# Performance work log

Measured on AMD Instinct MI355X. Metric: run time of the kernel, lower is better.

## Reference

```python
import jax, jax.numpy as jnp
import numpy as np

N_ATOMS = 131072
N_EDGES = 1048576  # avg degree 8
D = 64             # atom_state_dim
H = 64             # hidden width of all MLPs
OUT = 16           # output_dim
ATOMS_PER_MOL = 32
N_MOLS = N_ATOMS // ATOMS_PER_MOL  # 4096


def setup_inputs() -> dict:
    key = jax.random.key(0)
    ks = jax.random.split(key, 16)

    def lin(k, fan_in, fan_out):
        kw, kb = jax.random.split(k)
        bound = 1.0 / np.sqrt(fan_in)
        w = jax.random.uniform(kw, (fan_in, fan_out), jnp.float32, -bound, bound)
        b = jax.random.uniform(kb, (fan_out,), jnp.float32, -bound, bound)
        return w, b

    atom_states = jax.random.normal(ks[0], (N_ATOMS, D), jnp.float32)
    edge_src = jax.random.randint(ks[1], (N_EDGES,), 0, N_ATOMS, jnp.int32)
    edge_dst = jax.random.randint(ks[2], (N_EDGES,), 0, N_ATOMS, jnp.int32)
    atom_seg = (jnp.arange(N_ATOMS, dtype=jnp.int32) // ATOMS_PER_MOL)

    ms0_w, ms0_b = lin(ks[3], 2 * D, H)   # message MLP: 2d -> 64
    ms1_w, ms1_b = lin(ks[4], H, H)       # 64 -> 64
    ms2_w, ms2_b = lin(ks[5], H, D)       # 64 -> d
    fc1_w, fc1_b = lin(ks[6], D, H)       # readout: d -> 64
    fc2_w, fc2_b = lin(ks[7], H, H)       # 64 -> 64
    out_w, out_b = lin(ks[8], H, OUT)     # 64 -> output_dim

    return dict(atom_states=atom_states, edge_src=edge_src, edge_dst=edge_dst,
                atom_seg=atom_seg,
                ms0_w=ms0_w, ms0_b=ms0_b, ms1_w=ms1_w, ms1_b=ms1_b,
                ms2_w=ms2_w, ms2_b=ms2_b, fc1_w=fc1_w, fc1_b=fc1_b,
                fc2_w=fc2_w, fc2_b=fc2_b, out_w=out_w, out_b=out_b)


def reference(atom_states, edge_src, edge_dst, atom_seg,
              ms0_w, ms0_b, ms1_w, ms1_b, ms2_w, ms2_b,
              fc1_w, fc1_b, fc2_w, fc2_b, out_w, out_b):
    # per-edge feature: concat(state[dst_atom], state[neighbor])  -> [E, 2d]
    edge_feat = jnp.concatenate(
        [atom_states[edge_dst], atom_states[edge_src]], axis=-1)
    # message MLP (relu after every layer, as in the torch code)
    m = jax.nn.relu(edge_feat @ ms0_w + ms0_b)
    m = jax.nn.relu(m @ ms1_w + ms1_b)
    m = jax.nn.relu(m @ ms2_w + ms2_b)            # [E, d]
    # sum of incoming messages per atom (torch: stack(messages).sum(0))
    new_states = jax.ops.segment_sum(m, edge_dst, num_segments=N_ATOMS)  # [n_atoms, d]
    # readout MLP applied per atom
    h = jax.nn.relu(new_states @ fc1_w + fc1_b)
    h = jax.nn.relu(h @ fc2_w + fc2_b)
    o = jax.nn.relu(h @ out_w + out_b)            # [n_atoms, out]
    # sum over atoms within each molecule
    return jax.ops.segment_sum(o, atom_seg, num_segments=N_MOLS)  # [n_mols, out]
```

## Files before the change

kernel.cpp:

```cpp
#include <hip/hip_runtime.h>


constexpr int N_ATOMS = 131072;
constexpr int N_EDGES = 1048576;
constexpr int DD      = 64;
constexpr int OUTD    = 16;
constexpr int SH      = 72;
constexpr int SY      = 68;
constexpr int BCAP    = 16;
constexpr int OVF_CAP = 65536;

typedef __bf16 bf16x8 __attribute__((ext_vector_type(8)));
typedef float  f32x4  __attribute__((ext_vector_type(4)));
typedef unsigned short u16x8 __attribute__((ext_vector_type(8)));

#define DEV_INLINE __device__ __forceinline__

DEV_INLINE float relu(float x) { return x > 0.f ? x : 0.f; }

DEV_INLINE unsigned short bfbits(float x) {
  __bf16 h = (__bf16)x;
  return __builtin_bit_cast(unsigned short, h);
}
DEV_INLINE float bfval(unsigned short u) {
  unsigned int v = ((unsigned int)u) << 16;
  return __builtin_bit_cast(float, v);
}
DEV_INLINE f32x4 mfma16(bf16x8 a, bf16x8 b, f32x4 c) {
  return __builtin_amdgcn_mfma_f32_16x16x32_bf16(a, b, c, 0, 0, 0);
}
DEV_INLINE bf16x8 ldfrag(const unsigned short* p) { return *(const bf16x8*)p; }

DEV_INLINE void mk_frag(float4 a0, float4 a1, bf16x8& fh, bf16x8& fl) {
  const float v[8] = {a0.x, a0.y, a0.z, a0.w, a1.x, a1.y, a1.z, a1.w};
  u16x8 hh, ll;
#pragma unroll
  for (int i = 0; i < 8; ++i) {
    unsigned short h = bfbits(v[i]);
    hh[i] = h;
    ll[i] = bfbits(v[i] - bfval(h));
  }
  fh = __builtin_bit_cast(bf16x8, hh);
  fl = __builtin_bit_cast(bf16x8, ll);
}

DEV_INLINE void atom_pre_body(const float* __restrict__ atom_states,
                              const unsigned short* __restrict__ whi,
                              const unsigned short* __restrict__ wlo,
                              const float* __restrict__ b0,
                              float* __restrict__ Yd, float* __restrict__ Ys,
                              int a0, int t, float* st)
{
  const int l  = t & 63;
  const int w  = t >> 6;
  const int fi = (l >> 4) * 2;
  const int cc = l & 15;
  const int arow = a0 + w * 16 + (l & 15);

  bf16x8 xh[2], xl[2];
  {
    const float4* px = (const float4*)(atom_states + (size_t)arow * DD);
#pragma unroll
    for (int s = 0; s < 2; ++s) {
      float4 x0 = px[s * 8 + fi], x1 = px[s * 8 + fi + 1];
      mk_frag(x0, x1, xh[s], xl[s]);
    }
  }

#pragma unroll
  for (int side = 0; side < 2; ++side) {
    f32x4 acc[4];
#pragma unroll
    for (int j = 0; j < 4; ++j) acc[j] = (f32x4){0.f, 0.f, 0.f, 0.f};
#pragma unroll
    for (int s = 0; s < 2; ++s) {
#pragma unroll
      for (int j = 0; j < 4; ++j) {
        const int fo = side * 4096 + ((j * 2 + s) * 64 + l) * 8;
        bf16x8 bh = ldfrag(whi + fo);
        bf16x8 bl = ldfrag(wlo + fo);
        acc[j] = mfma16(xl[s], bh, acc[j]);
        acc[j] = mfma16(xh[s], bl, acc[j]);
        acc[j] = mfma16(xh[s], bh, acc[j]);
      }
    }
#pragma unroll
    for (int j = 0; j < 4; ++j) {
      const int   c  = j * 16 + cc;
      const float bb = side ? 0.f : b0[c];
#pragma unroll
      for (int i = 0; i < 4; ++i) {
        const int r = (l >> 4) * 4 + i;
        st[r * SY + c] = acc[j][i] + bb;
      }
    }
    {
      float* Y = side ? Ys : Yd;
      const int rr = l >> 2;
      const int c0 = (l & 3) * 16;
      float4* dst = (float4*)(Y + (size_t)(a0 + w * 16 + rr) * DD + c0);
      const float4* src = (const float4*)&st[rr * SY + c0];
#pragma unroll
      for (int f = 0; f < 4; ++f) dst[f] = src[f];
    }
  }
}

__global__ __launch_bounds__(256)
void k0_pack(const float* __restrict__ w0, const float* __restrict__ w1,
             const float* __restrict__ w2, const float* __restrict__ f1,
             const float* __restrict__ f2,
             unsigned short* __restrict__ whi, unsigned short* __restrict__ wlo)
{
  const int t = threadIdx.x, b = blockIdx.x;
  int tid = b * 256 + t;
  int sec = tid >> 9, rel = tid & 511;
  const float* w; int rowoff = 0;
  switch (sec) {
    case 0: w = w0; rowoff = 0;  break;
    case 1: w = w0; rowoff = 64; break;
    case 2: w = w1; break;
    case 3: w = w2; break;
    case 4: w = f1; break;
    default: w = f2; break;
  }
  const int tile = rel >> 6, lane = rel & 63;
  const int j = tile >> 1, s = tile & 1;
  const int n  = j * 16 + (lane & 15);
  const int kb = s * 32 + (lane >> 4) * 8;
  const int out = sec * 4096 + (tile * 64 + lane) * 8;
#pragma unroll
  for (int i = 0; i < 8; ++i) {
    float v = w[(rowoff + kb + i) * 64 + n];
    unsigned short h = bfbits(v);
    whi[out + i] = h;
    wlo[out + i] = bfbits(v - bfval(h));
  }
}

__global__ __launch_bounds__(256, 4)
void k1_bucket_pre(const float* __restrict__ atom_states,
                   const int* __restrict__ edge_src,
                   const int* __restrict__ edge_dst,
                   int* __restrict__ cnt, int* __restrict__ bucket,
                   int2* __restrict__ ovf, int* __restrict__ ovf_cnt,
                   const unsigned short* __restrict__ whi,
                   const unsigned short* __restrict__ wlo,
                   const float* __restrict__ b0,
                   float* __restrict__ Yd, float* __restrict__ Ys)
{
  __shared__ float Ystage[4][16 * SY];
  const int t = threadIdx.x, b = blockIdx.x;
  const int r3 = b % 3;
  if (r3 < 2) {
    int i = ((b / 3) * 2 + r3) * 256 + t;
    int d = edge_dst[i];
    int pos = atomicAdd(&cnt[d], 1);
    if (pos < BCAP) {
      bucket[d * BCAP + pos] = edge_src[i];
    } else {
      int op = atomicAdd(ovf_cnt, 1);
      if (op < OVF_CAP) ovf[op] = make_int2(d, edge_src[i]);
    }
    return;
  }
  atom_pre_body(atom_states, whi, wlo, b0, Yd, Ys, (b / 3) * 64, t,
                Ystage[t >> 6]);
}

__global__ __launch_bounds__(256, 4)
void k1_hist(const int* __restrict__ edge_dst, int* __restrict__ cnt) {
  int i = blockIdx.x * 256 + threadIdx.x;
  atomicAdd(&cnt[edge_dst[i]], 1);
}

__global__ void blocksum_kernel(const int* __restrict__ cnt,
                                int* __restrict__ partial, int clampv) {
  __shared__ int s[256];
  int t = threadIdx.x;
  s[t] = min(cnt[blockIdx.x * 256 + t], clampv);
  __syncthreads();
  for (int off = 128; off > 0; off >>= 1) {
    if (t < off) s[t] += s[t + off];
    __syncthreads();
  }
  if (t == 0) partial[blockIdx.x] = s[0];
}

__global__ void scanwrite_kernel(const int* __restrict__ cnt,
                                 const int* __restrict__ partial,
                                 int* __restrict__ cursor, int clampv) {
  __shared__ int s[256];
  __shared__ int pS[256];
  int t = threadIdx.x, b = blockIdx.x;

  int acc = 0;
  int p0 = partial[t];       if (t < b)       acc += p0;
  int p1 = partial[256 + t]; if (256 + t < b) acc += p1;
  pS[t] = acc;
  __syncthreads();
  for (int off = 128; off > 0; off >>= 1) {
    if (t < off) pS[t] += pS[t + off];
    __syncthreads();
  }
  const int base = pS[0];

  int v = min(cnt[b * 256 + t], clampv);
  s[t] = v;
  __syncthreads();
  for (int off = 1; off < 256; off <<= 1) {
    int x = (t >= off) ? s[t - off] : 0;
    __syncthreads();
    s[t] += x;
    __syncthreads();
  }
  cursor[b * 256 + t] = base + s[t] - v;
}

__global__ __launch_bounds__(256)
void scan_compact_kernel(const int* __restrict__ cnt,
                         const int* __restrict__ partial,
                         const int* __restrict__ bucket,
                         int2* __restrict__ ds_sorted) {
  __shared__ int s[256];
  __shared__ int pS[256];
  __shared__ int curS[256];
  __shared__ int vS[256];
  int t = threadIdx.x, b = blockIdx.x;

  int acc = 0;
  int p0 = partial[t];       if (t < b)       acc += p0;
  int p1 = partial[256 + t]; if (256 + t < b) acc += p1;
  pS[t] = acc;
  __syncthreads();
  for (int off = 128; off > 0; off >>= 1) {
    if (t < off) pS[t] += pS[t + off];
    __syncthreads();
  }
  const int base = pS[0];

  int v = min(cnt[b * 256 + t], BCAP);
  s[t] = v;
  __syncthreads();
  for (int off = 1; off < 256; off <<= 1) {
    int x = (t >= off) ? s[t - off] : 0;
    __syncthreads();
    s[t] += x;
    __syncthreads();
  }
  curS[t] = base + s[t] - v;
  vS[t]   = v;
  __syncthreads();

#pragma unroll
  for (int h = 0; h < 16; ++h) {
    const int j = h * 256 + t;
    const int al = j >> 4;
    const int slot = j & 15;
    if (slot < vS[al]) {
      const int a = b * 256 + al;
      ds_sorted[curS[al] + slot] = make_int2(a, bucket[a * BCAP + slot]);
    }
  }
}

__global__ __launch_bounds__(256, 4)
void k2_scatter_pre(const float* __restrict__ atom_states,
                    const int* __restrict__ edge_src,
                    const int* __restrict__ edge_dst,
                    int* __restrict__ cursor, int2* __restrict__ ds_sorted,
                    const unsigned short* __restrict__ whi,
                    const unsigned short* __restrict__ wlo,
                    const float* __restrict__ b0,
                    float* __restrict__ Yd, float* __restrict__ Ys)
{
  __shared__ float Ystage[4][16 * SY];
  const int t = threadIdx.x, b = blockIdx.x;
  const int r3 = b % 3;
  if (r3 < 2) {
    int i = ((b / 3) * 2 + r3) * 256 + t;
    int d = edge_dst[i];
    int pos = atomicAdd(&cursor[d], 1);
    ds_sorted[pos] = make_int2(d, edge_src[i]);
    return;
  }
  atom_pre_body(atom_states, whi, wlo, b0, Yd, Ys, (b / 3) * 64, t,
                Ystage[t >> 6]);
}

__global__ __launch_bounds__(256, 4)
void edge_kernel_v7c(const float* __restrict__ Yd,
                     const float* __restrict__ Ys,
                     const int2* __restrict__ ds_sorted,
                     const int* __restrict__ ovf_cnt,
                     const unsigned short* __restrict__ whi,
                     const unsigned short* __restrict__ wlo,
                     const float* __restrict__ b1,
                     const float* __restrict__ b2,
                     float* __restrict__ new_states)
{
  __shared__ __align__(16) unsigned short H2[4][2 * 32 * SH];

  const int t = threadIdx.x;
  const int w = t >> 6;
  const int l = t & 63;
  const int e0 = blockIdx.x * 128 + w * 32;

  const int total = N_EDGES - min(*ovf_cnt, OVF_CAP);
  const int n = min(max(total - e0, 0), 32);
  if (n <= 0) return;

  unsigned short* h2 = H2[w];
  float* msg = (float*)H2[w];

  int d = 0, s = 0;
  if (l < 32 && e0 + l < total) {
    int2 ds = ds_sorted[e0 + l];
    d = ds.x; s = ds.y;
  }

  const int m  = l & 15;
  const int fi = (l >> 4) * 2;
  const int cc = l & 15;

  bf16x8 a1h[2][2], a1l[2][2];
#pragma unroll
  for (int tile = 0; tile < 2; ++tile) {
    const int dm = __shfl(d, tile * 16 + m);
    const int sm = __shfl(s, tile * 16 + m);
    const float4* pd = (const float4*)(Yd + (size_t)dm * DD);
    const float4* ps = (const float4*)(Ys + (size_t)sm * DD);
#pragma unroll
    for (int s2 = 0; s2 < 2; ++s2) {
      float4 x0 = pd[s2 * 8 + fi], x1 = pd[s2 * 8 + fi + 1];
      float4 y0 = ps[s2 * 8 + fi], y1 = ps[s2 * 8 + fi + 1];
      float4 r0 = make_float4(relu(x0.x + y0.x), relu(x0.y + y0.y),
                              relu(x0.z + y0.z), relu(x0.w + y0.w));
      float4 r1 = make_float4(relu(x1.x + y1.x), relu(x1.y + y1.y),
                              relu(x1.z + y1.z), relu(x1.w + y1.w));
      mk_frag(r0, r1, a1h[tile][s2], a1l[tile][s2]);
    }
  }

  f32x4 acc[2][4];

#pragma unroll
  for (int tile = 0; tile < 2; ++tile)
#pragma unroll
    for (int j = 0; j < 4; ++j) acc[tile][j] = (f32x4){0.f, 0.f, 0.f, 0.f};
#pragma unroll
  for (int s2 = 0; s2 < 2; ++s2) {
#pragma unroll
    for (int j = 0; j < 4; ++j) {
      const int fo = 2 * 4096 + ((j * 2 + s2) * 64 + l) * 8;
      bf16x8 bh = ldfrag(whi + fo);
      bf16x8 bl = ldfrag(wlo + fo);
#pragma unroll
      for (int tile = 0; tile < 2; ++tile) {
        acc[tile][j] = mfma16(a1l[tile][s2], bh, acc[tile][j]);
        acc[tile][j] = mfma16(a1h[tile][s2], bl, acc[tile][j]);
        acc[tile][j] = mfma16(a1h[tile][s2], bh, acc[tile][j]);
      }
    }
  }
#pragma unroll
  for (int tile = 0; tile < 2; ++tile) {
#pragma unroll
    for (int j = 0; j < 4; ++j) {
      const int   c  = j * 16 + cc;
      const float bb = b1[c];
#pragma unroll
      for (int i = 0; i < 4; ++i) {
        const int r = tile * 16 + (l >> 4) * 4 + i;
        float v = relu(acc[tile][j][i] + bb);
        unsigned short hi = bfbits(v);
        h2[r * SH + c] = hi;
        h2[32 * SH + r * SH + c] = bfbits(v - bfval(hi));
      }
    }
  }

#pragma unroll
  for (int tile = 0; tile < 2; ++tile)
#pragma unroll
    for (int j = 0; j < 4; ++j) acc[tile][j] = (f32x4){0.f, 0.f, 0.f, 0.f};
  const int kq = (l >> 4) * 8;
#pragma unroll
  for (int s2 = 0; s2 < 2; ++s2) {
    bf16x8 ah[2], al[2];
#pragma unroll
    for (int tile = 0; tile < 2; ++tile) {
      const int mrow = tile * 16 + m;
      ah[tile] = ldfrag(&h2[mrow * SH + s2 * 32 + kq]);
      al[tile] = ldfrag(&h2[32 * SH + mrow * SH + s2 * 32 + kq]);
    }
#pragma unroll
    for (int j = 0; j < 4; ++j) {
      const int fo = 3 * 4096 + ((j * 2 + s2) * 64 + l) * 8;
      bf16x8 bh = ldfrag(whi + fo);
      bf16x8 bl = ldfrag(wlo + fo);
#pragma unroll
      for (int tile = 0; tile < 2; ++tile) {
        acc[tile][j] = mfma16(al[tile], bh, acc[tile][j]);
        acc[tile][j] = mfma16(ah[tile], bl, acc[tile][j]);
        acc[tile][j] = mfma16(ah[tile], bh, acc[tile][j]);
      }
    }
  }
#pragma unroll
  for (int tile = 0; tile < 2; ++tile) {
#pragma unroll
    for (int j = 0; j < 4; ++j) {
      const int   c  = j * 16 + cc;
      const float bb = b2[c];
#pragma unroll
      for (int i = 0; i < 4; ++i) {
        const int r = tile * 16 + (l >> 4) * 4 + i;
        msg[r * SH + c] = relu(acc[tile][j][i] + bb);
      }
    }
  }

  if (n == 32) {
    int   cur   = __builtin_amdgcn_readlane(d, 0);
    float run   = 0.f;
    bool  first = true;
#pragma unroll
    for (int r = 0; r < 32; ++r) {
      float v  = msg[r * SH + l];
      int   dr = __builtin_amdgcn_readlane(d, r);
      if (r > 0 && dr != cur) {
        float* p = new_states + (size_t)cur * DD + l;
        if (first) atomicAdd(p, run);
        else       *p = run;
        first = false;
        run = 0.f;
        cur = dr;
      }
      run += v;
    }
    atomicAdd(new_states + (size_t)cur * DD + l, run);
  } else {
    int   cur   = __builtin_amdgcn_readlane(d, 0);
    float run   = 0.f;
    bool  first = true;
    for (int r = 0; r < n; ++r) {
      float v  = msg[r * SH + l];
      int   dr = __builtin_amdgcn_readlane(d, r);
      if (r > 0 && dr != cur) {
        float* p = new_states + (size_t)cur * DD + l;
        if (first) atomicAdd(p, run);
        else       *p = run;
        first = false;
        run = 0.f;
        cur = dr;
      }
      run += v;
    }
    atomicAdd(new_states + (size_t)cur * DD + l, run);
  }
}

__global__ __launch_bounds__(256, 4)
void ovf_kernel(const float* __restrict__ Yd, const float* __restrict__ Ys,
                const float* __restrict__ w1, const float* __restrict__ b1,
                const float* __restrict__ w2, const float* __restrict__ b2,
                const int2* __restrict__ ovf, const int* __restrict__ ovf_cnt,
                float* __restrict__ new_states)
{
  __shared__ float hb[4][64];
  const int t = threadIdx.x;
  const int w = t >> 6;
  const int l = t & 63;
  const int wid = blockIdx.x * 4 + w;
  const int NW  = gridDim.x * 4;

  const int n = min(*ovf_cnt, OVF_CAP);
  for (int e = wid; e < n; e += NW) {
    int2 ds = ovf[e];
    float h1 = relu(Yd[(size_t)ds.x * DD + l] + Ys[(size_t)ds.y * DD + l]);
    hb[w][l] = h1;
    float acc = 0.f;
#pragma unroll 8
    for (int k = 0; k < 64; ++k) acc += hb[w][k] * w1[k * 64 + l];
    float h2 = relu(acc + b1[l]);
    hb[w][l] = h2;
    acc = 0.f;
#pragma unroll 8
    for (int k = 0; k < 64; ++k) acc += hb[w][k] * w2[k * 64 + l];
    atomicAdd(&new_states[(size_t)ds.x * DD + l], relu(acc + b2[l]));
  }
}

__global__ __launch_bounds__(256, 4)
void atom_kernel_v2(const float* __restrict__ ns,
                    const unsigned short* __restrict__ whi,
                    const unsigned short* __restrict__ wlo,
                    const float* __restrict__ f1b,
                    const float* __restrict__ f2b,
                    const float* __restrict__ wo,
                    const float* __restrict__ bo,
                    float* __restrict__ out)
{
  __shared__ __align__(16) unsigned short Xb[2 * 64 * SH];
  __shared__ __align__(16) unsigned short Hb[2 * 64 * SH];
  unsigned short* Xh = Xb;
  unsigned short* Xl = Xb + 64 * SH;
  unsigned short* Hh = Hb;
  unsigned short* Hl = Hb + 64 * SH;
  float* h2f = (float*)Xb;
  float* oS  = (float*)Hb;

  const int t  = threadIdx.x;
  const int a0 = blockIdx.x * 64;

  {
    const int r  = t >> 2;
    const int k0 = (t & 3) * 16;
    const float4* s4 = (const float4*)(ns + (size_t)(a0 + r) * DD + k0);
#pragma unroll
    for (int f = 0; f < 4; ++f) {
      float4 v = s4[f];
      ushort4 h, lo;
      h.x = bfbits(v.x); lo.x = bfbits(v.x - bfval(h.x));
      h.y = bfbits(v.y); lo.y = bfbits(v.y - bfval(h.y));
      h.z = bfbits(v.z); lo.z = bfbits(v.z - bfval(h.z));
      h.w = bfbits(v.w); lo.w = bfbits(v.w - bfval(h.w));
      *(ushort4*)&Xh[r * SH + k0 + f * 4] = h;
      *(ushort4*)&Xl[r * SH + k0 + f * 4] = lo;
    }
  }

  const int l    = t & 63;
  const int w    = t >> 6;
  const int mrow = w * 16 + (l & 15);
  const int kq   = (l >> 4) * 8;
  const int cc   = l & 15;

  f32x4 acc[4];

#pragma unroll
  for (int j = 0; j < 4; ++j) acc[j] = (f32x4){0.f, 0.f, 0.f, 0.f};
#pragma unroll
  for (int s = 0; s < 2; ++s) {
    bf16x8 ah = ldfrag(&Xh[mrow * SH + s * 32 + kq]);
    bf16x8 al = ldfrag(&Xl[mrow * SH + s * 32 + kq]);
#pragma unroll
    for (int j = 0; j < 4; ++j) {
      const int fo = 4 * 4096 + ((j * 2 + s) * 64 + l) * 8;
      bf16x8 bh = ldfrag(whi + fo);
      bf16x8 bl = ldfrag(wlo + fo);
      acc[j] = mfma16(al, bh, acc[j]);
      acc[j] = mfma16(ah, bl, acc[j]);
      acc[j] = mfma16(ah, bh, acc[j]);
    }
  }
#pragma unroll
  for (int j = 0; j < 4; ++j) {
    const int   c  = j * 16 + cc;
    const float bb = f1b[c];
#pragma unroll
    for (int i = 0; i < 4; ++i) {
      const int r = w * 16 + (l >> 4) * 4 + i;
      float v = relu(acc[j][i] + bb);
      unsigned short hi = bfbits(v);
      Hh[r * SH + c] = hi;
      Hl[r * SH + c] = bfbits(v - bfval(hi));
    }
  }
  __syncthreads();

#pragma unroll
  for (int j = 0; j < 4; ++j) acc[j] = (f32x4){0.f, 0.f, 0.f, 0.f};
#pragma unroll
  for (int s = 0; s < 2; ++s) {
    bf16x8 ah = ldfrag(&Hh[mrow * SH + s * 32 + kq]);
    bf16x8 al = ldfrag(&Hl[mrow * SH + s * 32 + kq]);
#pragma unroll
    for (int j = 0; j < 4; ++j) {
      const int fo = 5 * 4096 + ((j * 2 + s) * 64 + l) * 8;
      bf16x8 bh = ldfrag(whi + fo);
      bf16x8 bl = ldfrag(wlo + fo);
      acc[j] = mfma16(al, bh, acc[j]);
      acc[j] = mfma16(ah, bl, acc[j]);
      acc[j] = mfma16(ah, bh, acc[j]);
    }
  }
#pragma unroll
  for (int j = 0; j < 4; ++j) {
    const int   c  = j * 16 + cc;
    const float bb = f2b[c];
#pragma unroll
    for (int i = 0; i < 4; ++i) {
      const int r = w * 16 + (l >> 4) * 4 + i;
      h2f[r * SH + c] = relu(acc[j][i] + bb);
    }
  }
  __syncthreads();

  {
    const int r  = t >> 2;
    const int c4 = (t & 3) * 4;
    float o4[4] = {0.f, 0.f, 0.f, 0.f};
#pragma unroll 8
    for (int k = 0; k < 64; ++k) {
      const float a = h2f[r * SH + k];
      float4 bw = *(const float4*)&wo[k * OUTD + c4];
      o4[0] += a * bw.x; o4[1] += a * bw.y; o4[2] += a * bw.z; o4[3] += a * bw.w;
    }
#pragma unroll
    for (int j = 0; j < 4; ++j)
      oS[r * 17 + c4 + j] = relu(o4[j] + bo[c4 + j]);
  }
  __syncthreads();

  if (t < 32) {
    const int m = t >> 4;
    const int c = t & 15;
    float s = 0.f;
#pragma unroll
    for (int a = 0; a < 32; ++a) s += oS[(m * 32 + a) * 17 + c];
    out[(blockIdx.x * 2 + m) * OUTD + c] = s;
  }
}

extern "C" void kernel_launch(void* const* d_in, const int* in_sizes, int n_in,
                              void* d_out, int out_size, void* d_ws, size_t ws_size,
                              hipStream_t stream) {
  const float* atom_states = (const float*)d_in[0];
  const int*   edge_src    = (const int*)d_in[1];
  const int*   edge_dst    = (const int*)d_in[2];
  const float* ms0_w = (const float*)d_in[4];
  const float* ms0_b = (const float*)d_in[5];
  const float* ms1_w = (const float*)d_in[6];
  const float* ms1_b = (const float*)d_in[7];
  const float* ms2_w = (const float*)d_in[8];
  const float* ms2_b = (const float*)d_in[9];
  const float* fc1_w = (const float*)d_in[10];
  const float* fc1_b = (const float*)d_in[11];
  const float* fc2_w = (const float*)d_in[12];
  const float* fc2_b = (const float*)d_in[13];
  const float* out_w = (const float*)d_in[14];
  const float* out_b = (const float*)d_in[15];

  char* ws = (char*)d_ws;
  float* new_states = (float*)ws;
  size_t off = (size_t)N_ATOMS * DD * sizeof(float);
  int* cnt     = (int*)(ws + off); off += (size_t)N_ATOMS * 4;
  int* cursor  = (int*)(ws + off); off += (size_t)N_ATOMS * 4;
  int* partial = (int*)(ws + off); off += 4096;
  int* ovf_cnt = (int*)(ws + off); off += 4096;
  int2* ovf    = (int2*)(ws + off); off += (size_t)OVF_CAP * 8;
  unsigned short* whi = (unsigned short*)(ws + off); off += 24576 * 2;
  unsigned short* wlo = (unsigned short*)(ws + off); off += 24576 * 2;
  float* Yd = (float*)(ws + off); off += (size_t)N_ATOMS * DD * sizeof(float);
  float* Ys = (float*)(ws + off); off += (size_t)N_ATOMS * DD * sizeof(float);
  int2* ds_sorted = (int2*)(ws + off); off += (size_t)N_EDGES * 8;
  const size_t needB = off;
  int* bucket = (int*)(ws + off); off += (size_t)N_ATOMS * BCAP * 4;
  const size_t needC = off;

  const int useC = (ws_size >= needC) ? 1 : 0;

  hipMemsetAsync(new_states, 0, (size_t)N_ATOMS * DD * sizeof(float), stream);
  hipMemsetAsync(cnt, 0, (size_t)N_ATOMS * 4, stream);
  hipMemsetAsync(ovf_cnt, 0, 4, stream);

  k0_pack<<<12, 256, 0, stream>>>(ms0_w, ms1_w, ms2_w, fc1_w, fc2_w, whi, wlo);

  if (useC) {
    k1_bucket_pre<<<6144, 256, 0, stream>>>(atom_states, edge_src, edge_dst,
                                            cnt, bucket, ovf, ovf_cnt,
                                            whi, wlo, ms0_b, Yd, Ys);
    blocksum_kernel<<<512, 256, 0, stream>>>(cnt, partial, BCAP);
    scan_compact_kernel<<<512, 256, 0, stream>>>(cnt, partial, bucket, ds_sorted);
  } else {
    k1_hist<<<4096, 256, 0, stream>>>(edge_dst, cnt);
    blocksum_kernel<<<512, 256, 0, stream>>>(cnt, partial, 0x7fffffff);
    scanwrite_kernel<<<512, 256, 0, stream>>>(cnt, partial, cursor, 0x7fffffff);
    k2_scatter_pre<<<6144, 256, 0, stream>>>(atom_states, edge_src, edge_dst,
                                             cursor, ds_sorted,
                                             whi, wlo, ms0_b, Yd, Ys);
  }

  edge_kernel_v7c<<<N_EDGES / 128, 256, 0, stream>>>(
      Yd, Ys, ds_sorted, ovf_cnt, whi, wlo, ms1_b, ms2_b, new_states);

  if (useC) {
    ovf_kernel<<<64, 256, 0, stream>>>(Yd, Ys, ms1_w, ms1_b, ms2_w, ms2_b,
                                       ovf, ovf_cnt, new_states);
  }

  atom_kernel_v2<<<N_ATOMS / 64, 256, 0, stream>>>(
      new_states, whi, wlo, fc1_b, fc2_b, out_w, out_b, (float*)d_out);
}
```

Before: 325.5 us.

## Fold overflow edges into sorted list and replace block scan with atomic base

Overflow edges whose destination bucket is full are now written directly into the tail of the sorted edge array, so the edge kernel handles them and the separate scalar overflow kernel is removed. The two-pass block-sum plus scan is replaced by a single kernel in which each block claims its output offset with one global atomicAdd, dropping a launch. The edge kernel always processes full 32-edge groups and uses atomics for every segment flush instead of plain stores for interior segments. Atomic base ordering makes block output positions nondeterministic, and segments of one destination can be split across groups, which the atomics still handle correctly.

```diff
diff --git a/kernel.cpp b/kernel.cpp
--- a/kernel.cpp
+++ b/kernel.cpp
@@ -8,7 +8,6 @@
 constexpr int SH      = 72;
 constexpr int SY      = 68;
 constexpr int BCAP    = 16;
-constexpr int OVF_CAP = 65536;
 
 typedef __bf16 bf16x8 __attribute__((ext_vector_type(8)));
 typedef float  f32x4  __attribute__((ext_vector_type(4)));
@@ -143,7 +142,7 @@
                    const int* __restrict__ edge_src,
                    const int* __restrict__ edge_dst,
                    int* __restrict__ cnt, int* __restrict__ bucket,
-                   int2* __restrict__ ovf, int* __restrict__ ovf_cnt,
+                   int2* __restrict__ ds_sorted, int* __restrict__ ovf_cnt,
                    const unsigned short* __restrict__ whi,
                    const unsigned short* __restrict__ wlo,
                    const float* __restrict__ b0,
@@ -160,7 +159,7 @@
       bucket[d * BCAP + pos] = edge_src[i];
     } else {
       int op = atomicAdd(ovf_cnt, 1);
-      if (op < OVF_CAP) ovf[op] = make_int2(d, edge_src[i]);
+      ds_sorted[N_EDGES - 1 - op] = make_int2(d, edge_src[i]);
     }
     return;
   }
@@ -218,26 +217,15 @@
 }
 
 __global__ __launch_bounds__(256)
-void scan_compact_kernel(const int* __restrict__ cnt,
-                         const int* __restrict__ partial,
+void scan_compact_atomic(const int* __restrict__ cnt,
+                         int* __restrict__ gbase,
                          const int* __restrict__ bucket,
                          int2* __restrict__ ds_sorted) {
   __shared__ int s[256];
-  __shared__ int pS[256];
   __shared__ int curS[256];
   __shared__ int vS[256];
+  __shared__ int baseS;
   int t = threadIdx.x, b = blockIdx.x;
-
-  int acc = 0;
-  int p0 = partial[t];       if (t < b)       acc += p0;
-  int p1 = partial[256 + t]; if (256 + t < b) acc += p1;
-  pS[t] = acc;
-  __syncthreads();
-  for (int off = 128; off > 0; off >>= 1) {
-    if (t < off) pS[t] += pS[t + off];
-    __syncthreads();
-  }
-  const int base = pS[0];
 
   int v = min(cnt[b * 256 + t], BCAP);
   s[t] = v;
@@ -248,7 +236,9 @@
     s[t] += x;
     __syncthreads();
   }
-  curS[t] = base + s[t] - v;
+  if (t == 255) baseS = atomicAdd(gbase, s[255]);
+  __syncthreads();
+  curS[t] = baseS + s[t] - v;
   vS[t]   = v;
   __syncthreads();
 
@@ -289,10 +279,9 @@
 }
 
 __global__ __launch_bounds__(256, 4)
-void edge_kernel_v7c(const float* __restrict__ Yd,
+void edge_kernel_v10(const float* __restrict__ Yd,
                      const float* __restrict__ Ys,
                      const int2* __restrict__ ds_sorted,
-                     const int* __restrict__ ovf_cnt,
                      const unsigned short* __restrict__ whi,
                      const unsigned short* __restrict__ wlo,
                      const float* __restrict__ b1,
@@ -306,15 +295,11 @@
   const int l = t & 63;
   const int e0 = blockIdx.x * 128 + w * 32;
 
-  const int total = N_EDGES - min(*ovf_cnt, OVF_CAP);
-  const int n = min(max(total - e0, 0), 32);
-  if (n <= 0) return;
-
   unsigned short* h2 = H2[w];
   float* msg = (float*)H2[w];
 
   int d = 0, s = 0;
-  if (l < 32 && e0 + l < total) {
+  if (l < 32) {
     int2 ds = ds_sorted[e0 + l];
     d = ds.x; s = ds.y;
   }
@@ -421,74 +406,21 @@
     }
   }
 
-  if (n == 32) {
-    int   cur   = __builtin_amdgcn_readlane(d, 0);
-    float run   = 0.f;
-    bool  first = true;
+  {
+    int   cur = __builtin_amdgcn_readlane(d, 0);
+    float run = 0.f;
 #pragma unroll
     for (int r = 0; r < 32; ++r) {
       float v  = msg[r * SH + l];
       int   dr = __builtin_amdgcn_readlane(d, r);
       if (r > 0 && dr != cur) {
-        float* p = new_states + (size_t)cur * DD + l;
-        if (first) atomicAdd(p, run);
-        else       *p = run;
-        first = false;
+        atomicAdd(new_states + (size_t)cur * DD + l, run);
         run = 0.f;
         cur = dr;
       }
       run += v;
     }
     atomicAdd(new_states + (size_t)cur * DD + l, run);
-  } else {
-    int   cur   = __builtin_amdgcn_readlane(d, 0);
-    float run   = 0.f;
-    bool  first = true;
-    for (int r = 0; r < n; ++r) {
-      float v  = msg[r * SH + l];
-      int   dr = __builtin_amdgcn_readlane(d, r);
-      if (r > 0 && dr != cur) {
-        float* p = new_states + (size_t)cur * DD + l;
-        if (first) atomicAdd(p, run);
-        else       *p = run;
-        first = false;
-        run = 0.f;
-        cur = dr;
-      }
-      run += v;
-    }
-    atomicAdd(new_states + (size_t)cur * DD + l, run);
-  }
-}
-
-__global__ __launch_bounds__(256, 4)
-void ovf_kernel(const float* __restrict__ Yd, const float* __restrict__ Ys,
-                const float* __restrict__ w1, const float* __restrict__ b1,
-                const float* __restrict__ w2, const float* __restrict__ b2,
-                const int2* __restrict__ ovf, const int* __restrict__ ovf_cnt,
-                float* __restrict__ new_states)
-{
-  __shared__ float hb[4][64];
-  const int t = threadIdx.x;
-  const int w = t >> 6;
-  const int l = t & 63;
-  const int wid = blockIdx.x * 4 + w;
-  const int NW  = gridDim.x * 4;
-
-  const int n = min(*ovf_cnt, OVF_CAP);
-  for (int e = wid; e < n; e += NW) {
-    int2 ds = ovf[e];
-    float h1 = relu(Yd[(size_t)ds.x * DD + l] + Ys[(size_t)ds.y * DD + l]);
-    hb[w][l] = h1;
-    float acc = 0.f;
-#pragma unroll 8
-    for (int k = 0; k < 64; ++k) acc += hb[w][k] * w1[k * 64 + l];
-    float h2 = relu(acc + b1[l]);
-    hb[w][l] = h2;
-    acc = 0.f;
-#pragma unroll 8
-    for (int k = 0; k < 64; ++k) acc += hb[w][k] * w2[k * 64 + l];
-    atomicAdd(&new_states[(size_t)ds.x * DD + l], relu(acc + b2[l]));
   }
 }
 
@@ -649,8 +581,8 @@
   int* cnt     = (int*)(ws + off); off += (size_t)N_ATOMS * 4;
   int* cursor  = (int*)(ws + off); off += (size_t)N_ATOMS * 4;
   int* partial = (int*)(ws + off); off += 4096;
-  int* ovf_cnt = (int*)(ws + off); off += 4096;
-  int2* ovf    = (int2*)(ws + off); off += (size_t)OVF_CAP * 8;
+  int* ovf_cnt = (int*)(ws + off); off += 2048;
+  int* gbase   = (int*)(ws + off); off += 2048;
   unsigned short* whi = (unsigned short*)(ws + off); off += 24576 * 2;
   unsigned short* wlo = (unsigned short*)(ws + off); off += 24576 * 2;
   float* Yd = (float*)(ws + off); off += (size_t)N_ATOMS * DD * sizeof(float);
@@ -665,15 +597,15 @@
   hipMemsetAsync(new_states, 0, (size_t)N_ATOMS * DD * sizeof(float), stream);
   hipMemsetAsync(cnt, 0, (size_t)N_ATOMS * 4, stream);
   hipMemsetAsync(ovf_cnt, 0, 4, stream);
+  hipMemsetAsync(gbase, 0, 4, stream);
 
   k0_pack<<<12, 256, 0, stream>>>(ms0_w, ms1_w, ms2_w, fc1_w, fc2_w, whi, wlo);
 
   if (useC) {
     k1_bucket_pre<<<6144, 256, 0, stream>>>(atom_states, edge_src, edge_dst,
-                                            cnt, bucket, ovf, ovf_cnt,
+                                            cnt, bucket, ds_sorted, ovf_cnt,
                                             whi, wlo, ms0_b, Yd, Ys);
-    blocksum_kernel<<<512, 256, 0, stream>>>(cnt, partial, BCAP);
-    scan_compact_kernel<<<512, 256, 0, stream>>>(cnt, partial, bucket, ds_sorted);
+    scan_compact_atomic<<<512, 256, 0, stream>>>(cnt, gbase, bucket, ds_sorted);
   } else {
     k1_hist<<<4096, 256, 0, stream>>>(edge_dst, cnt);
     blocksum_kernel<<<512, 256, 0, stream>>>(cnt, partial, 0x7fffffff);
@@ -683,13 +615,8 @@
                                              whi, wlo, ms0_b, Yd, Ys);
   }
 
-  edge_kernel_v7c<<<N_EDGES / 128, 256, 0, stream>>>(
-      Yd, Ys, ds_sorted, ovf_cnt, whi, wlo, ms1_b, ms2_b, new_states);
-
-  if (useC) {
-    ovf_kernel<<<64, 256, 0, stream>>>(Yd, Ys, ms1_w, ms1_b, ms2_w, ms2_b,
-                                       ovf, ovf_cnt, new_states);
-  }
+  edge_kernel_v10<<<N_EDGES / 128, 256, 0, stream>>>(
+      Yd, Ys, ds_sorted, whi, wlo, ms1_b, ms2_b, new_states);
 
   atom_kernel_v2<<<N_ATOMS / 64, 256, 0, stream>>>(
       new_states, whi, wlo, fc1_b, fc2_b, out_w, out_b, (float*)d_out);
```

After: 309.9 us. -4.8%, faster.
